# Kernel tuning notes

Measured on AMD Instinct MI355X. Metric: run time of the kernel, lower is better.

## Reference

```python
import jax, jax.numpy as jnp
import numpy as np

NHEAD = 16
EPS_L1 = 1e-12
LN_EPS = 1e-5


def _layernorm(x, g, b):
    mu = jnp.mean(x, axis=-1, keepdims=True)
    var = jnp.mean(jnp.square(x - mu), axis=-1, keepdims=True)
    return (x - mu) / jnp.sqrt(var + LN_EPS) * g + b


def setup_inputs() -> dict:
    key = jax.random.key(0)
    ks = jax.random.split(key, 16)
    S, B, E, P, F = 2048, 2, 1024, 64, 4096
    sc = lambda n: 1.0 / np.sqrt(n)
    return {
        "src": jax.random.normal(ks[0], (S, B, E), jnp.float32),
        "pos_embed": jax.random.normal(ks[1], (B, P, S), jnp.float32),
        "in_proj_w": jax.random.normal(ks[2], (3 * E, E), jnp.float32) * sc(E),
        "in_proj_b": jnp.zeros((3 * E,), jnp.float32),
        "out_w": jax.random.normal(ks[3], (E, E), jnp.float32) * sc(E),
        "out_b": jnp.zeros((E,), jnp.float32),
        "lin1_w": jax.random.normal(ks[4], (F, E), jnp.float32) * sc(E),
        "lin1_b": jnp.zeros((F,), jnp.float32),
        "lin2_w": jax.random.normal(ks[5], (E, F), jnp.float32) * sc(F),
        "lin2_b": jnp.zeros((E,), jnp.float32),
        "ln1_g": jnp.ones((E,), jnp.float32),
        "ln1_b": jnp.zeros((E,), jnp.float32),
        "ln2_g": jnp.ones((E,), jnp.float32),
        "ln2_b": jnp.zeros((E,), jnp.float32),
        "pos_w": jax.random.normal(ks[6], (P, P), jnp.float32) * sc(P),
        "pos_b": jnp.zeros((P,), jnp.float32),
    }


def reference(src, pos_embed, in_proj_w, in_proj_b, out_w, out_b,
              lin1_w, lin1_b, lin2_w, lin2_b,
              ln1_g, ln1_b, ln2_g, ln2_b, pos_w, pos_b):
    S, B, E = src.shape
    H = NHEAD
    Dh = E // H

    # --- custom positional-similarity kernel (cosine_similarity w/ L1 norm) ---
    pe = jnp.einsum('bps,qp->bqs', pos_embed, pos_w) + pos_b[None, :, None]  # learnable pos
    l1 = jnp.maximum(jnp.sum(jnp.abs(pe), axis=1, keepdims=True), EPS_L1)
    pe = pe / l1                                                # [B,P,S]
    pos_sim = jnp.einsum('bps,bpt->bst', pe, pe)                # [B,S,S]

    # --- manual multi-head self-attention ---
    qkv = src @ in_proj_w.T + in_proj_b                          # [S,B,3E]
    q, k, v = jnp.split(qkv, 3, axis=-1)
    q = q * (Dh ** -0.5)
    to_bhsd = lambda t: jnp.transpose(t.reshape(S, B, H, Dh), (1, 2, 0, 3))
    q, k, v = to_bhsd(q), to_bhsd(k), to_bhsd(v)                 # [B,H,S,Dh]
    scores = jnp.einsum('bhsd,bhtd->bhst', q, k) + pos_sim[:, None]
    attn = jax.nn.softmax(scores, axis=-1)                       # [B,H,S,S]
    ctx = jnp.einsum('bhst,bhtd->bhsd', attn, v)                 # [B,H,S,Dh]
    ctx = jnp.transpose(ctx, (2, 0, 1, 3)).reshape(S, B, E)
    attn_out = ctx @ out_w.T + out_b

    # --- residual + norm + FFN (post-norm, relu) ---
    x = _layernorm(src + attn_out, ln1_g, ln1_b)
    ff = jax.nn.relu(x @ lin1_w.T + lin1_b) @ lin2_w.T + lin2_b
    return _layernorm(x + ff, ln2_g, ln2_b)
```

## Files before the change

kernel.cpp:

```cpp
#include <hip/hip_runtime.h>
#include <hip/hip_bf16.h>
#include <math.h>

#define S_LEN 2048
#define BATCH 2
#define EMB   1024
#define NH    16
#define DH    64
#define E3    3072
#define FF    4096
#define PP    64

typedef __bf16 bf16x8 __attribute__((ext_vector_type(8)));
typedef float  floatx4 __attribute__((ext_vector_type(4)));

__device__ __forceinline__ void load_lds16(const void* g, void* l) {
  __builtin_amdgcn_global_load_lds(
      (const __attribute__((address_space(1))) void*)g,
      (__attribute__((address_space(3))) void*)l, 16, 0, 0);
}

__global__ __launch_bounds__(256) void cvt5_kernel(
    const float* __restrict__ in0, __hip_bfloat16* __restrict__ o0,
    const float* __restrict__ in1, __hip_bfloat16* __restrict__ o1,
    const float* __restrict__ in2, __hip_bfloat16* __restrict__ o2,
    const float* __restrict__ in3, __hip_bfloat16* __restrict__ o3,
    const float* __restrict__ in4, __hip_bfloat16* __restrict__ o4)
{
  int bid = blockIdx.x;
  const float* in; __hip_bfloat16* out; int base;
  if      (bid < 2048) { in = in0; out = o0; base = bid; }
  else if (bid < 3584) { in = in1; out = o1; base = bid - 2048; }
  else if (bid < 4096) { in = in2; out = o2; base = bid - 3584; }
  else if (bid < 6144) { in = in3; out = o3; base = bid - 4096; }
  else                 { in = in4; out = o4; base = bid - 6144; }
  int i = (base * 256 + threadIdx.x) * 8;
  float4 a = *(const float4*)&in[i];
  float4 b = *(const float4*)&in[i + 4];
  __hip_bfloat16 t[8];
  t[0] = __float2bfloat16(a.x); t[1] = __float2bfloat16(a.y);
  t[2] = __float2bfloat16(a.z); t[3] = __float2bfloat16(a.w);
  t[4] = __float2bfloat16(b.x); t[5] = __float2bfloat16(b.y);
  t[6] = __float2bfloat16(b.z); t[7] = __float2bfloat16(b.w);
  *(float4*)&out[i] = *(float4*)t;
}

__global__ __launch_bounds__(64) void pe_kernel(
    const float* __restrict__ pos_embed, const float* __restrict__ pos_w,
    const float* __restrict__ pos_b, __hip_bfloat16* __restrict__ peT)
{
  __shared__ float pw[PP * PP];
  int tid = threadIdx.x;
  for (int i = 0; i < PP; ++i) pw[i * PP + tid] = pos_w[i * PP + tid];
  __syncthreads();
  int s = blockIdx.x * 64 + tid;
  int b = blockIdx.y;
  float acc[PP];
#pragma unroll
  for (int q = 0; q < PP; ++q) acc[q] = pos_b[q];
  for (int p = 0; p < PP; ++p) {
    float x = pos_embed[(size_t)(b * PP + p) * S_LEN + s];
#pragma unroll
    for (int q = 0; q < PP; ++q) acc[q] += pw[q * PP + p] * x;
  }
  float l1 = 0.f;
#pragma unroll
  for (int q = 0; q < PP; ++q) l1 += fabsf(acc[q]);
  float inv = 1.f / fmaxf(l1, 1e-12f);
  __hip_bfloat16 tmp[PP];
#pragma unroll
  for (int q = 0; q < PP; ++q) tmp[q] = __float2bfloat16(acc[q] * inv);
  float4* dst = (float4*)&peT[((size_t)b * S_LEN + s) * PP];
#pragma unroll
  for (int i = 0; i < 8; ++i) dst[i] = ((float4*)tmp)[i];
}

template <int WR, int WC>
__global__ __launch_bounds__(256) void gemm_bf16(
    const __hip_bfloat16* __restrict__ A, const __hip_bfloat16* __restrict__ W,
    const float* __restrict__ bias, float* __restrict__ Cf,
    __hip_bfloat16* __restrict__ Cb, int M, int N, int K, int relu, int qkscale,
    long strideA, long strideW, long strideC)
{
  constexpr int BM = 2 * WR * 16;
  constexpr int BN = 2 * WC * 16;
  __shared__ __bf16 As[BM * 64];
  __shared__ __bf16 Bs[BN * 64];
  A += (size_t)blockIdx.z * strideA;
  W += (size_t)blockIdx.z * strideW;
  int tid = threadIdx.x;
  int bm = blockIdx.y * BM;
  int bn = blockIdx.x * BN;
  int wave = tid >> 6, lane = tid & 63;
  int wm = (wave & 1) * (WR * 16), wn = (wave >> 1) * (WC * 16);
  int srow = tid >> 3, scb = tid & 7;
  int gcb = scb ^ (srow & 7);
  const __hip_bfloat16* Ap = A + (size_t)(bm + srow) * K + gcb * 8;
  const __hip_bfloat16* Wp = W + (size_t)(bn + srow) * K + gcb * 8;
  __bf16* AsBase = As + tid * 8;
  __bf16* BsBase = Bs + tid * 8;
  int r15 = lane & 15, quad = lane >> 4;

  floatx4 acc[WR * WC];
#pragma unroll
  for (int i = 0; i < WR * WC; ++i) acc[i] = (floatx4){0.f, 0.f, 0.f, 0.f};

  for (int k0 = 0; k0 < K; k0 += 64) {
    __syncthreads();
#pragma unroll
    for (int io = 0; io < BM / 32; ++io)
      load_lds16(Ap + (size_t)(32 * io) * K + k0, AsBase + io * 2048);
#pragma unroll
    for (int io = 0; io < BN / 32; ++io)
      load_lds16(Wp + (size_t)(32 * io) * K + k0, BsBase + io * 2048);
    __syncthreads();
#pragma unroll
    for (int kc = 0; kc < 2; ++kc) {
      bf16x8 af[WR], bfv[WC];
      int kb = kc * 4 + quad;
#pragma unroll
      for (int i = 0; i < WR; ++i) {
        int rowa = wm + i * 16 + r15;
        af[i] = *(const bf16x8*)&As[rowa * 64 + (kb ^ (rowa & 7)) * 8];
      }
#pragma unroll
      for (int j = 0; j < WC; ++j) {
        int rowb = wn + j * 16 + r15;
        bfv[j] = *(const bf16x8*)&Bs[rowb * 64 + (kb ^ (rowb & 7)) * 8];
      }
#pragma unroll
      for (int i = 0; i < WR; ++i)
#pragma unroll
        for (int j = 0; j < WC; ++j)
          acc[i * WC + j] = __builtin_amdgcn_mfma_f32_16x16x32_bf16(
              af[i], bfv[j], acc[i * WC + j], 0, 0, 0);
    }
  }
  int crow0 = bm + wm + quad * 4;
  int ccol0 = bn + wn + r15;
  float* CfB = Cf ? Cf + (size_t)blockIdx.z * strideC : nullptr;
  __hip_bfloat16* CbB = Cb ? Cb + (size_t)blockIdx.z * strideC : nullptr;
#pragma unroll
  for (int j = 0; j < WC; ++j) {
    int col = ccol0 + j * 16;
    float bv = bias ? bias[col] : 0.f;
    float scale = (qkscale && col < EMB) ? 0.125f : 1.f;
#pragma unroll
    for (int i = 0; i < WR; ++i) {
#pragma unroll
      for (int r = 0; r < 4; ++r) {
        int row = crow0 + i * 16 + r;
        float v = (acc[i * WC + j][r] + bv) * scale;
        if (relu) v = fmaxf(v, 0.f);
        if (CfB) CfB[(size_t)row * N + col] = v;
        if (CbB) CbB[(size_t)row * N + col] = __float2bfloat16(v);
      }
    }
  }
}

__global__ __launch_bounds__(512, 2) void gemm256_bf16(
    const __hip_bfloat16* __restrict__ A, const __hip_bfloat16* __restrict__ W,
    const float* __restrict__ bias, __hip_bfloat16* __restrict__ Cb,
    int M, int N, int K, int relu, int qkscale)
{
  __shared__ __bf16 As[2][16384];
  __shared__ __bf16 Bs[2][16384];
  const int tid = threadIdx.x;
  const int bm = blockIdx.y * 256;
  const int bn = blockIdx.x * 256;
  const int wave = tid >> 6, lane = tid & 63;
  const int wm = (wave >> 2) * 128, wn = (wave & 3) * 64;
  const int r15 = lane & 15, quad = lane >> 4;
  const int srow = tid >> 3, scb = tid & 7;
  const int NT = K >> 6;

  const __hip_bfloat16* Ap = A + (size_t)bm * K;
  const __hip_bfloat16* Wp = W + (size_t)bn * K;

  auto stageA = [&](int buf, int k0, int h) {
#pragma unroll
    for (int io = 0; io < 2; ++io) {
      int row = h * 128 + io * 64 + srow;
      int gcb = scb ^ (row & 7);
      load_lds16(Ap + (size_t)row * K + k0 + gcb * 8,
                 &As[buf][(h * 128 + io * 64) * 64] + tid * 8);
    }
  };
  auto stageB = [&](int buf, int k0, int h) {
#pragma unroll
    for (int io = 0; io < 2; ++io) {
      int row = h * 128 + io * 64 + srow;
      int gcb = scb ^ (row & 7);
      load_lds16(Wp + (size_t)row * K + k0 + gcb * 8,
                 &Bs[buf][(h * 128 + io * 64) * 64] + tid * 8);
    }
  };

  floatx4 acc[8][4];
#pragma unroll
  for (int i = 0; i < 8; ++i)
#pragma unroll
    for (int jn = 0; jn < 4; ++jn) acc[i][jn] = (floatx4){0.f, 0.f, 0.f, 0.f};

  stageA(0, 0, 0); stageA(0, 0, 1);
  stageB(0, 0, 0); stageB(0, 0, 1);
  stageA(1, 64, 0); stageA(1, 64, 1);
  asm volatile("s_waitcnt vmcnt(4)" ::: "memory");
  __builtin_amdgcn_s_barrier();
  __builtin_amdgcn_sched_barrier(0);

#define PHASE_BAR() do { __builtin_amdgcn_sched_barrier(0); \
                         __builtin_amdgcn_s_barrier();      \
                         __builtin_amdgcn_sched_barrier(0); } while (0)

  bf16x8 af[4][2], bfr[4][2];
  for (int j = 0; j < NT; ++j) {
    const int cur = j & 1, nxt = cur ^ 1;
    const int k1 = (j + 1) << 6, k2 = (j + 2) << 6;

#pragma unroll
    for (int i = 0; i < 4; ++i) {
      int row = wm + i * 16 + r15;
#pragma unroll
      for (int kc = 0; kc < 2; ++kc)
        af[i][kc] = *(const bf16x8*)&As[cur][row * 64 + (((kc * 4 + quad) ^ (row & 7)) * 8)];
    }
#pragma unroll
    for (int jn = 0; jn < 2; ++jn) {
      int row = wn + jn * 16 + r15;
#pragma unroll
      for (int kc = 0; kc < 2; ++kc)
        bfr[jn][kc] = *(const bf16x8*)&Bs[cur][row * 64 + (((kc * 4 + quad) ^ (row & 7)) * 8)];
    }
    if (j + 1 < NT) stageB(nxt, k1, 0);
    PHASE_BAR();
    __builtin_amdgcn_s_setprio(1);
#pragma unroll
    for (int i = 0; i < 4; ++i)
#pragma unroll
      for (int jn = 0; jn < 2; ++jn)
#pragma unroll
        for (int kc = 0; kc < 2; ++kc)
          acc[i][jn] = __builtin_amdgcn_mfma_f32_16x16x32_bf16(
              af[i][kc], bfr[jn][kc], acc[i][jn], 0, 0, 0);
    __builtin_amdgcn_s_setprio(0);
    PHASE_BAR();

#pragma unroll
    for (int jn = 2; jn < 4; ++jn) {
      int row = wn + jn * 16 + r15;
#pragma unroll
      for (int kc = 0; kc < 2; ++kc)
        bfr[jn][kc] = *(const bf16x8*)&Bs[cur][row * 64 + (((kc * 4 + quad) ^ (row & 7)) * 8)];
    }
    if (j + 1 < NT) stageB(nxt, k1, 1);
    PHASE_BAR();
    __builtin_amdgcn_s_setprio(1);
#pragma unroll
    for (int i = 0; i < 4; ++i)
#pragma unroll
      for (int jn = 2; jn < 4; ++jn)
#pragma unroll
        for (int kc = 0; kc < 2; ++kc)
          acc[i][jn] = __builtin_amdgcn_mfma_f32_16x16x32_bf16(
              af[i][kc], bfr[jn][kc], acc[i][jn], 0, 0, 0);
    __builtin_amdgcn_s_setprio(0);
    PHASE_BAR();

#pragma unroll
    for (int i = 0; i < 4; ++i) {
      int row = wm + (i + 4) * 16 + r15;
#pragma unroll
      for (int kc = 0; kc < 2; ++kc)
        af[i][kc] = *(const bf16x8*)&As[cur][row * 64 + (((kc * 4 + quad) ^ (row & 7)) * 8)];
    }
    PHASE_BAR();
    __builtin_amdgcn_s_setprio(1);
#pragma unroll
    for (int i = 0; i < 4; ++i)
#pragma unroll
      for (int jn = 2; jn < 4; ++jn)
#pragma unroll
        for (int kc = 0; kc < 2; ++kc)
          acc[i + 4][jn] = __builtin_amdgcn_mfma_f32_16x16x32_bf16(
              af[i][kc], bfr[jn][kc], acc[i + 4][jn], 0, 0, 0);
    __builtin_amdgcn_s_setprio(0);
    PHASE_BAR();

    if (j + 2 < NT) { stageA(cur, k2, 0); stageA(cur, k2, 1); }
    if (j < NT - 2) asm volatile("s_waitcnt vmcnt(4)" ::: "memory");
    else            asm volatile("s_waitcnt vmcnt(0)" ::: "memory");
    PHASE_BAR();
    __builtin_amdgcn_s_setprio(1);
#pragma unroll
    for (int i = 0; i < 4; ++i)
#pragma unroll
      for (int jn = 0; jn < 2; ++jn)
#pragma unroll
        for (int kc = 0; kc < 2; ++kc)
          acc[i + 4][jn] = __builtin_amdgcn_mfma_f32_16x16x32_bf16(
              af[i][kc], bfr[jn][kc], acc[i + 4][jn], 0, 0, 0);
    __builtin_amdgcn_s_setprio(0);
    PHASE_BAR();
  }
#undef PHASE_BAR

  const int crow0 = bm + wm + quad * 4;
  const int ccol0 = bn + wn + r15;
#pragma unroll
  for (int jn = 0; jn < 4; ++jn) {
    int col = ccol0 + jn * 16;
    float bv = bias ? bias[col] : 0.f;
    float scale = (qkscale && col < EMB) ? 0.125f : 1.f;
#pragma unroll
    for (int i = 0; i < 8; ++i) {
#pragma unroll
      for (int r = 0; r < 4; ++r) {
        int row = crow0 + i * 16 + r;
        float v = (acc[i][jn][r] + bv) * scale;
        if (relu) v = fmaxf(v, 0.f);
        Cb[(size_t)row * N + col] = __float2bfloat16(v);
      }
    }
  }
}

__global__ __launch_bounds__(256) void transpose_v(
    const __hip_bfloat16* __restrict__ qkv, __hip_bfloat16* __restrict__ vT)
{
  __shared__ __hip_bfloat16 tile[64][72];
  int c0 = blockIdx.x * 64, t0 = blockIdx.y * 64, b = blockIdx.z;
  int tid = threadIdx.x;
#pragma unroll
  for (int i = 0; i < 2; ++i) {
    int k = tid * 2 + i;
    int row = k >> 3, col = (k & 7) * 8;
    float4 v = *(const float4*)&qkv[((size_t)(t0 + row) * BATCH + b) * E3 + 2 * EMB + c0 + col];
    __hip_bfloat16 tmp[8];
    *(float4*)tmp = v;
#pragma unroll
    for (int j = 0; j < 8; ++j) tile[row][col + j] = tmp[j];
  }
  __syncthreads();
#pragma unroll
  for (int i = 0; i < 2; ++i) {
    int k = tid * 2 + i;
    int crow = k >> 3, tcol = (k & 7) * 8;
    __hip_bfloat16 tmp[8];
#pragma unroll
    for (int j = 0; j < 8; ++j) tmp[j] = tile[tcol + j][crow];
    *(float4*)&vT[((size_t)(b * EMB + c0 + crow)) * S_LEN + t0 + tcol] = *(float4*)tmp;
  }
}

__global__ __launch_bounds__(512, 4) void attn_mfma(
    const __hip_bfloat16* __restrict__ qkv,
    const __hip_bfloat16* __restrict__ vT,
    const __hip_bfloat16* __restrict__ peT,
    __hip_bfloat16* __restrict__ ctx)
{
  __shared__ __bf16 Ks[2][4096];
  __shared__ __bf16 Kp[2][4096];
  __shared__ __bf16 Vs[2][4096];
  __shared__ __bf16 Ps[8192];
  int tid = threadIdx.x;
  int q0 = blockIdx.x * 128, h = blockIdx.y, b = blockIdx.z;
  int w = tid >> 6, lane = tid & 63, quad = lane >> 4, r15 = lane & 15;
  int srow = tid >> 3, scb = tid & 7;
  int x7 = r15 & 7;

  const __hip_bfloat16* kbase = qkv + EMB + (size_t)h * DH;
  const __hip_bfloat16* vbase = vT + ((size_t)b * EMB + h * DH) * S_LEN;
  const __hip_bfloat16* pbase = peT + (size_t)b * S_LEN * PP;

  bf16x8 qa[4];
  {
    int qrow = q0 + w * 16 + r15;
#pragma unroll
    for (int kc = 0; kc < 2; ++kc)
      qa[kc] = *(const bf16x8*)&qkv[
          ((size_t)qrow * BATCH + b) * E3 + h * DH + kc * 32 + quad * 8];
#pragma unroll
    for (int kc = 0; kc < 2; ++kc)
      qa[2 + kc] = *(const bf16x8*)&pbase[
          (size_t)qrow * PP + kc * 32 + quad * 8];
  }

  {
    int row = srow;
    int gcb = scb ^ (row & 7);
    load_lds16(kbase + ((size_t)row * BATCH + b) * E3 + gcb * 8, Ks[0] + tid * 8);
    load_lds16(pbase + (size_t)row * PP + gcb * 8, Kp[0] + tid * 8);
    load_lds16(vbase + (size_t)row * S_LEN + gcb * 8, Vs[0] + tid * 8);
  }
  __syncthreads();

  floatx4 of[4];
#pragma unroll
  for (int j = 0; j < 4; ++j) of[j] = (floatx4){0.f, 0.f, 0.f, 0.f};
  float lp = 0.f;

  __bf16* pw = Ps + w * 1024;

  for (int kt = 0; kt < 32; ++kt) {
    int cur = kt & 1;
    int t0 = kt * 64;
    if (kt < 31) {
      int tn = t0 + 64;
      int nb = cur ^ 1;
      int row = srow;
      int gcb = scb ^ (row & 7);
      load_lds16(kbase + ((size_t)(tn + row) * BATCH + b) * E3 + gcb * 8,
                 Ks[nb] + tid * 8);
      load_lds16(pbase + (size_t)(tn + row) * PP + gcb * 8,
                 Kp[nb] + tid * 8);
      load_lds16(vbase + (size_t)row * S_LEN + tn + gcb * 8,
                 Vs[nb] + tid * 8);
    }

    floatx4 sf[4];
#pragma unroll
    for (int j = 0; j < 4; ++j) sf[j] = (floatx4){0.f, 0.f, 0.f, 0.f};
#pragma unroll
    for (int j = 0; j < 4; ++j) {
      int rowk = j * 16 + r15;
      int rx = rowk & 7;
      bf16x8 kf0 = *(const bf16x8*)&Ks[cur][rowk * 64 + ((quad ^ rx)) * 8];
      bf16x8 kf1 = *(const bf16x8*)&Ks[cur][rowk * 64 + (((4 + quad) ^ rx)) * 8];
      bf16x8 kp0 = *(const bf16x8*)&Kp[cur][rowk * 64 + ((quad ^ rx)) * 8];
      bf16x8 kp1 = *(const bf16x8*)&Kp[cur][rowk * 64 + (((4 + quad) ^ rx)) * 8];
      sf[j] = __builtin_amdgcn_mfma_f32_16x16x32_bf16(kf0, qa[0], sf[j], 0, 0, 0);
      sf[j] = __builtin_amdgcn_mfma_f32_16x16x32_bf16(kf1, qa[1], sf[j], 0, 0, 0);
      sf[j] = __builtin_amdgcn_mfma_f32_16x16x32_bf16(kp0, qa[2], sf[j], 0, 0, 0);
      sf[j] = __builtin_amdgcn_mfma_f32_16x16x32_bf16(kp1, qa[3], sf[j], 0, 0, 0);
    }

#pragma unroll
    for (int j = 0; j < 4; ++j) {
      float e0 = __expf(fminf(sf[j][0], 60.f));
      float e1 = __expf(fminf(sf[j][1], 60.f));
      float e2 = __expf(fminf(sf[j][2], 60.f));
      float e3 = __expf(fminf(sf[j][3], 60.f));
      lp += (e0 + e1) + (e2 + e3);
      __hip_bfloat16 t4[4];
      t4[0] = __float2bfloat16(e0); t4[1] = __float2bfloat16(e1);
      t4[2] = __float2bfloat16(e2); t4[3] = __float2bfloat16(e3);
      int addr = r15 * 64 + (((j * 2 + (quad >> 1)) ^ x7) * 8) + (quad & 1) * 4;
      *(float2*)&pw[addr] = *(float2*)t4;
    }
    __asm__ volatile("s_waitcnt lgkmcnt(0)" ::: "memory");

    bf16x8 pb0 = *(const bf16x8*)&pw[r15 * 64 + ((quad ^ x7) * 8)];
    bf16x8 pb1 = *(const bf16x8*)&pw[r15 * 64 + (((4 + quad) ^ x7) * 8)];
#pragma unroll
    for (int jd = 0; jd < 4; ++jd) {
      int rowd = jd * 16 + r15;
      bf16x8 vb0 = *(const bf16x8*)&Vs[cur][rowd * 64 + (quad ^ (rowd & 7)) * 8];
      bf16x8 vb1 = *(const bf16x8*)&Vs[cur][rowd * 64 + ((4 + quad) ^ (rowd & 7)) * 8];
      of[jd] = __builtin_amdgcn_mfma_f32_16x16x32_bf16(vb0, pb0, of[jd], 0, 0, 0);
      of[jd] = __builtin_amdgcn_mfma_f32_16x16x32_bf16(vb1, pb1, of[jd], 0, 0, 0);
    }
    __syncthreads();
  }

  {
    float l = lp;
    l += __shfl_xor(l, 16, 64);
    l += __shfl_xor(l, 32, 64);
    float inv = 1.f / l;
    size_t rbase = ((size_t)(q0 + w * 16 + r15) * BATCH + b) * EMB + h * DH;
#pragma unroll
    for (int jd = 0; jd < 4; ++jd) {
      __hip_bfloat16 o4[4];
      o4[0] = __float2bfloat16(of[jd][0] * inv);
      o4[1] = __float2bfloat16(of[jd][1] * inv);
      o4[2] = __float2bfloat16(of[jd][2] * inv);
      o4[3] = __float2bfloat16(of[jd][3] * inv);
      *(float2*)&ctx[rbase + jd * 16 + quad * 4] = *(float2*)o4;
    }
  }
}

__global__ __launch_bounds__(256) void ln_kernel(
    const float* __restrict__ x1, const float* __restrict__ x2,
    const float* __restrict__ g, const float* __restrict__ bb,
    float* __restrict__ out, __hip_bfloat16* __restrict__ out_bf)
{
  int row = blockIdx.x;
  int tid = threadIdx.x;
  const float* p1 = x1 + (size_t)row * EMB;
  const float* p2 = x2 + (size_t)row * EMB;
  float4 v1 = *(const float4*)&p1[tid * 4];
  float4 v2 = *(const float4*)&p2[tid * 4];
  float x[4] = {v1.x + v2.x, v1.y + v2.y, v1.z + v2.z, v1.w + v2.w};
  float s = x[0] + x[1] + x[2] + x[3];
  float s2 = x[0] * x[0] + x[1] * x[1] + x[2] * x[2] + x[3] * x[3];
#pragma unroll
  for (int off = 32; off >= 1; off >>= 1) {
    s  += __shfl_xor(s, off, 64);
    s2 += __shfl_xor(s2, off, 64);
  }
  __shared__ float ws1[4], ws2[4];
  int wid = tid >> 6, lane = tid & 63;
  if (lane == 0) { ws1[wid] = s; ws2[wid] = s2; }
  __syncthreads();
  s  = ws1[0] + ws1[1] + ws1[2] + ws1[3];
  s2 = ws2[0] + ws2[1] + ws2[2] + ws2[3];
  float mean = s * (1.f / EMB);
  float var  = s2 * (1.f / EMB) - mean * mean;
  float inv  = rsqrtf(var + 1e-5f);
  float4 gv = *(const float4*)&g[tid * 4];
  float4 bv = *(const float4*)&bb[tid * 4];
  float4 o;
  o.x = (x[0] - mean) * inv * gv.x + bv.x;
  o.y = (x[1] - mean) * inv * gv.y + bv.y;
  o.z = (x[2] - mean) * inv * gv.z + bv.z;
  o.w = (x[3] - mean) * inv * gv.w + bv.w;
  *(float4*)&out[(size_t)row * EMB + tid * 4] = o;
  if (out_bf) {
    __hip_bfloat16 t[4];
    t[0] = __float2bfloat16(o.x); t[1] = __float2bfloat16(o.y);
    t[2] = __float2bfloat16(o.z); t[3] = __float2bfloat16(o.w);
    *(float2*)&out_bf[(size_t)row * EMB + tid * 4] = *(float2*)t;
  }
}

extern "C" void kernel_launch(void* const* d_in, const int* in_sizes, int n_in,
                              void* d_out, int out_size, void* d_ws, size_t ws_size,
                              hipStream_t stream)
{
  const float* src       = (const float*)d_in[0];
  const float* pos_embed = (const float*)d_in[1];
  const float* in_proj_w = (const float*)d_in[2];
  const float* in_proj_b = (const float*)d_in[3];
  const float* out_w     = (const float*)d_in[4];
  const float* out_b     = (const float*)d_in[5];
  const float* lin1_w    = (const float*)d_in[6];
  const float* lin1_b    = (const float*)d_in[7];
  const float* lin2_w    = (const float*)d_in[8];
  const float* lin2_b    = (const float*)d_in[9];
  const float* ln1_g     = (const float*)d_in[10];
  const float* ln1_b     = (const float*)d_in[11];
  const float* ln2_g     = (const float*)d_in[12];
  const float* ln2_b     = (const float*)d_in[13];
  const float* pos_w     = (const float*)d_in[14];
  const float* pos_b     = (const float*)d_in[15];
  float* out = (float*)d_out;
  float* ws  = (float*)d_ws;

  __hip_bfloat16* peT    = (__hip_bfloat16*)ws;
  __hip_bfloat16* qkv_bf = (__hip_bfloat16*)(ws + 8519680);
  __hip_bfloat16* vT_bf  = (__hip_bfloat16*)(ws + 14811136);
  __hip_bfloat16* src_bf = (__hip_bfloat16*)(ws + 16908288);
  __hip_bfloat16* inw_bf  = (__hip_bfloat16*)(ws + 19005440);
  __hip_bfloat16* outw_bf = (__hip_bfloat16*)(ws + 20578304);
  __hip_bfloat16* ctx_bf = (__hip_bfloat16*)(ws + 21102592);
  __hip_bfloat16* l1w_bf = (__hip_bfloat16*)(ws + 23199744);
  __hip_bfloat16* l2w_bf = (__hip_bfloat16*)(ws + 25296896);
  float* proj            = ws + 27394048;
  __hip_bfloat16* x_bf   = (__hip_bfloat16*)ws;
  float* xbuf            = ws + 2097152;
  __hip_bfloat16* h1_bf  = (__hip_bfloat16*)(ws + 6291456);

  const int M = S_LEN * BATCH;

  cvt5_kernel<<<8192, 256, 0, stream>>>(
      src, src_bf, in_proj_w, inw_bf, out_w, outw_bf,
      lin1_w, l1w_bf, lin2_w, l2w_bf);
  pe_kernel<<<dim3(S_LEN / 64, BATCH), 64, 0, stream>>>(pos_embed, pos_w, pos_b, peT);
  gemm256_bf16<<<dim3(E3 / 256, M / 256), 512, 0, stream>>>(
      src_bf, inw_bf, in_proj_b, qkv_bf, M, E3, EMB, 0, 1);
  transpose_v<<<dim3(EMB / 64, S_LEN / 64, BATCH), 256, 0, stream>>>(qkv_bf, vT_bf);
  attn_mfma<<<dim3(S_LEN / 128, NH, BATCH), 512, 0, stream>>>(
      qkv_bf, vT_bf, peT, ctx_bf);
  gemm_bf16<2, 4><<<dim3(EMB / 128, M / 64, 1), 256, 0, stream>>>(
      ctx_bf, outw_bf, out_b, proj, nullptr, M, EMB, EMB, 0, 0, 0, 0, 0);
  ln_kernel<<<dim3(M), 256, 0, stream>>>(src, proj, ln1_g, ln1_b, xbuf, x_bf);
  gemm256_bf16<<<dim3(FF / 256, M / 256), 512, 0, stream>>>(
      x_bf, l1w_bf, lin1_b, h1_bf, M, FF, EMB, 1, 0);
  gemm_bf16<2, 4><<<dim3(EMB / 128, M / 64, 1), 256, 0, stream>>>(
      h1_bf, l2w_bf, lin2_b, proj, nullptr, M, EMB, FF, 0, 0, 0, 0, 0);
  ln_kernel<<<dim3(M), 256, 0, stream>>>(xbuf, proj, ln2_g, ln2_b, out, nullptr);
}
```

Measured before the change: 405.8 us.

## Split-K lin2 GEMM with 3-way LN reduce and exp2-based attention softmax

The FFN second GEMM becomes a 2-way split-K with 128x128 tiles, writing two partial fp32 outputs. A new layernorm kernel sums the residual and both partials, which raises CU occupancy for the K=4096 GEMM at the cost of extra fp32 traffic. The attention softmax now uses exp2 with log2e folded into the Q scale and a pre-scaled positional embedding copy, and the overflow clamp is removed. s_setprio is also added around the MFMA blocks in attention.

```diff
diff --git a/kernel.cpp b/kernel.cpp
--- a/kernel.cpp
+++ b/kernel.cpp
@@ -10,6 +10,8 @@
 #define E3    3072
 #define FF    4096
 #define PP    64
+#define QSCALE 0.18033688f
+#define LOG2E  1.4426950408889634f
 
 typedef __bf16 bf16x8 __attribute__((ext_vector_type(8)));
 typedef float  floatx4 __attribute__((ext_vector_type(4)));
@@ -47,7 +49,8 @@
 
 __global__ __launch_bounds__(64) void pe_kernel(
     const float* __restrict__ pos_embed, const float* __restrict__ pos_w,
-    const float* __restrict__ pos_b, __hip_bfloat16* __restrict__ peT)
+    const float* __restrict__ pos_b, __hip_bfloat16* __restrict__ peT,
+    __hip_bfloat16* __restrict__ peQ)
 {
   __shared__ float pw[PP * PP];
   int tid = threadIdx.x;
@@ -67,12 +70,17 @@
 #pragma unroll
   for (int q = 0; q < PP; ++q) l1 += fabsf(acc[q]);
   float inv = 1.f / fmaxf(l1, 1e-12f);
-  __hip_bfloat16 tmp[PP];
-#pragma unroll
-  for (int q = 0; q < PP; ++q) tmp[q] = __float2bfloat16(acc[q] * inv);
+  __hip_bfloat16 tmp[PP], tmq[PP];
+#pragma unroll
+  for (int q = 0; q < PP; ++q) {
+    float v = acc[q] * inv;
+    tmp[q] = __float2bfloat16(v);
+    tmq[q] = __float2bfloat16(v * LOG2E);
+  }
   float4* dst = (float4*)&peT[((size_t)b * S_LEN + s) * PP];
-#pragma unroll
-  for (int i = 0; i < 8; ++i) dst[i] = ((float4*)tmp)[i];
+  float4* dsq = (float4*)&peQ[((size_t)b * S_LEN + s) * PP];
+#pragma unroll
+  for (int i = 0; i < 8; ++i) { dst[i] = ((float4*)tmp)[i]; dsq[i] = ((float4*)tmq)[i]; }
 }
 
 template <int WR, int WC>
@@ -80,7 +88,7 @@
     const __hip_bfloat16* __restrict__ A, const __hip_bfloat16* __restrict__ W,
     const float* __restrict__ bias, float* __restrict__ Cf,
     __hip_bfloat16* __restrict__ Cb, int M, int N, int K, int relu, int qkscale,
-    long strideA, long strideW, long strideC)
+    int ldA, int ldW, long strideA, long strideW, long strideC)
 {
   constexpr int BM = 2 * WR * 16;
   constexpr int BN = 2 * WC * 16;
@@ -95,8 +103,8 @@
   int wm = (wave & 1) * (WR * 16), wn = (wave >> 1) * (WC * 16);
   int srow = tid >> 3, scb = tid & 7;
   int gcb = scb ^ (srow & 7);
-  const __hip_bfloat16* Ap = A + (size_t)(bm + srow) * K + gcb * 8;
-  const __hip_bfloat16* Wp = W + (size_t)(bn + srow) * K + gcb * 8;
+  const __hip_bfloat16* Ap = A + (size_t)(bm + srow) * ldA + gcb * 8;
+  const __hip_bfloat16* Wp = W + (size_t)(bn + srow) * ldW + gcb * 8;
   __bf16* AsBase = As + tid * 8;
   __bf16* BsBase = Bs + tid * 8;
   int r15 = lane & 15, quad = lane >> 4;
@@ -109,10 +117,10 @@
     __syncthreads();
 #pragma unroll
     for (int io = 0; io < BM / 32; ++io)
-      load_lds16(Ap + (size_t)(32 * io) * K + k0, AsBase + io * 2048);
+      load_lds16(Ap + (size_t)(32 * io) * ldA + k0, AsBase + io * 2048);
 #pragma unroll
     for (int io = 0; io < BN / 32; ++io)
-      load_lds16(Wp + (size_t)(32 * io) * K + k0, BsBase + io * 2048);
+      load_lds16(Wp + (size_t)(32 * io) * ldW + k0, BsBase + io * 2048);
     __syncthreads();
 #pragma unroll
     for (int kc = 0; kc < 2; ++kc) {
@@ -138,13 +146,13 @@
   }
   int crow0 = bm + wm + quad * 4;
   int ccol0 = bn + wn + r15;
-  float* CfB = Cf ? Cf + (size_t)blockIdx.z * strideC : nullptr;
-  __hip_bfloat16* CbB = Cb ? Cb + (size_t)blockIdx.z * strideC : nullptr;
+  float* CfB = Cf ? Cf + (long)blockIdx.z * strideC : nullptr;
+  __hip_bfloat16* CbB = Cb;
 #pragma unroll
   for (int j = 0; j < WC; ++j) {
     int col = ccol0 + j * 16;
-    float bv = bias ? bias[col] : 0.f;
-    float scale = (qkscale && col < EMB) ? 0.125f : 1.f;
+    float bv = (bias && blockIdx.z == 0) ? bias[col] : 0.f;
+    float scale = (qkscale && col < EMB) ? QSCALE : 1.f;
 #pragma unroll
     for (int i = 0; i < WR; ++i) {
 #pragma unroll
@@ -312,7 +320,7 @@
   for (int jn = 0; jn < 4; ++jn) {
     int col = ccol0 + jn * 16;
     float bv = bias ? bias[col] : 0.f;
-    float scale = (qkscale && col < EMB) ? 0.125f : 1.f;
+    float scale = (qkscale && col < EMB) ? QSCALE : 1.f;
 #pragma unroll
     for (int i = 0; i < 8; ++i) {
 #pragma unroll
@@ -358,6 +366,7 @@
     const __hip_bfloat16* __restrict__ qkv,
     const __hip_bfloat16* __restrict__ vT,
     const __hip_bfloat16* __restrict__ peT,
+    const __hip_bfloat16* __restrict__ peQ,
     __hip_bfloat16* __restrict__ ctx)
 {
   __shared__ __bf16 Ks[2][4096];
@@ -372,7 +381,8 @@
 
   const __hip_bfloat16* kbase = qkv + EMB + (size_t)h * DH;
   const __hip_bfloat16* vbase = vT + ((size_t)b * EMB + h * DH) * S_LEN;
-  const __hip_bfloat16* pbase = peT + (size_t)b * S_LEN * PP;
+  const __hip_bfloat16* pkbase = peT + (size_t)b * S_LEN * PP;
+  const __hip_bfloat16* pqbase = peQ + (size_t)b * S_LEN * PP;
 
   bf16x8 qa[4];
   {
@@ -383,7 +393,7 @@
           ((size_t)qrow * BATCH + b) * E3 + h * DH + kc * 32 + quad * 8];
 #pragma unroll
     for (int kc = 0; kc < 2; ++kc)
-      qa[2 + kc] = *(const bf16x8*)&pbase[
+      qa[2 + kc] = *(const bf16x8*)&pqbase[
           (size_t)qrow * PP + kc * 32 + quad * 8];
   }
 
@@ -391,7 +401,7 @@
     int row = srow;
     int gcb = scb ^ (row & 7);
     load_lds16(kbase + ((size_t)row * BATCH + b) * E3 + gcb * 8, Ks[0] + tid * 8);
-    load_lds16(pbase + (size_t)row * PP + gcb * 8, Kp[0] + tid * 8);
+    load_lds16(pkbase + (size_t)row * PP + gcb * 8, Kp[0] + tid * 8);
     load_lds16(vbase + (size_t)row * S_LEN + gcb * 8, Vs[0] + tid * 8);
   }
   __syncthreads();
@@ -413,7 +423,7 @@
       int gcb = scb ^ (row & 7);
       load_lds16(kbase + ((size_t)(tn + row) * BATCH + b) * E3 + gcb * 8,
                  Ks[nb] + tid * 8);
-      load_lds16(pbase + (size_t)(tn + row) * PP + gcb * 8,
+      load_lds16(pkbase + (size_t)(tn + row) * PP + gcb * 8,
                  Kp[nb] + tid * 8);
       load_lds16(vbase + (size_t)row * S_LEN + tn + gcb * 8,
                  Vs[nb] + tid * 8);
@@ -422,6 +432,7 @@
     floatx4 sf[4];
 #pragma unroll
     for (int j = 0; j < 4; ++j) sf[j] = (floatx4){0.f, 0.f, 0.f, 0.f};
+    __builtin_amdgcn_s_setprio(1);
 #pragma unroll
     for (int j = 0; j < 4; ++j) {
       int rowk = j * 16 + r15;
@@ -435,13 +446,14 @@
       sf[j] = __builtin_amdgcn_mfma_f32_16x16x32_bf16(kp0, qa[2], sf[j], 0, 0, 0);
       sf[j] = __builtin_amdgcn_mfma_f32_16x16x32_bf16(kp1, qa[3], sf[j], 0, 0, 0);
     }
+    __builtin_amdgcn_s_setprio(0);
 
 #pragma unroll
     for (int j = 0; j < 4; ++j) {
-      float e0 = __expf(fminf(sf[j][0], 60.f));
-      float e1 = __expf(fminf(sf[j][1], 60.f));
-      float e2 = __expf(fminf(sf[j][2], 60.f));
-      float e3 = __expf(fminf(sf[j][3], 60.f));
+      float e0 = exp2f(sf[j][0]);
+      float e1 = exp2f(sf[j][1]);
+      float e2 = exp2f(sf[j][2]);
+      float e3 = exp2f(sf[j][3]);
       lp += (e0 + e1) + (e2 + e3);
       __hip_bfloat16 t4[4];
       t4[0] = __float2bfloat16(e0); t4[1] = __float2bfloat16(e1);
@@ -453,6 +465,7 @@
 
     bf16x8 pb0 = *(const bf16x8*)&pw[r15 * 64 + ((quad ^ x7) * 8)];
     bf16x8 pb1 = *(const bf16x8*)&pw[r15 * 64 + (((4 + quad) ^ x7) * 8)];
+    __builtin_amdgcn_s_setprio(1);
 #pragma unroll
     for (int jd = 0; jd < 4; ++jd) {
       int rowd = jd * 16 + r15;
@@ -461,6 +474,7 @@
       of[jd] = __builtin_amdgcn_mfma_f32_16x16x32_bf16(vb0, pb0, of[jd], 0, 0, 0);
       of[jd] = __builtin_amdgcn_mfma_f32_16x16x32_bf16(vb1, pb1, of[jd], 0, 0, 0);
     }
+    __builtin_amdgcn_s_setprio(0);
     __syncthreads();
   }
 
@@ -526,6 +540,48 @@
   }
 }
 
+__global__ __launch_bounds__(256) void ln3_kernel(
+    const float* __restrict__ x1, const float* __restrict__ x2,
+    const float* __restrict__ x3,
+    const float* __restrict__ g, const float* __restrict__ bb,
+    float* __restrict__ out)
+{
+  int row = blockIdx.x;
+  int tid = threadIdx.x;
+  const float* p1 = x1 + (size_t)row * EMB;
+  const float* p2 = x2 + (size_t)row * EMB;
+  const float* p3 = x3 + (size_t)row * EMB;
+  float4 v1 = *(const float4*)&p1[tid * 4];
+  float4 v2 = *(const float4*)&p2[tid * 4];
+  float4 v3 = *(const float4*)&p3[tid * 4];
+  float x[4] = {v1.x + v2.x + v3.x, v1.y + v2.y + v3.y,
+                v1.z + v2.z + v3.z, v1.w + v2.w + v3.w};
+  float s = x[0] + x[1] + x[2] + x[3];
+  float s2 = x[0] * x[0] + x[1] * x[1] + x[2] * x[2] + x[3] * x[3];
+#pragma unroll
+  for (int off = 32; off >= 1; off >>= 1) {
+    s  += __shfl_xor(s, off, 64);
+    s2 += __shfl_xor(s2, off, 64);
+  }
+  __shared__ float ws1[4], ws2[4];
+  int wid = tid >> 6, lane = tid & 63;
+  if (lane == 0) { ws1[wid] = s; ws2[wid] = s2; }
+  __syncthreads();
+  s  = ws1[0] + ws1[1] + ws1[2] + ws1[3];
+  s2 = ws2[0] + ws2[1] + ws2[2] + ws2[3];
+  float mean = s * (1.f / EMB);
+  float var  = s2 * (1.f / EMB) - mean * mean;
+  float inv  = rsqrtf(var + 1e-5f);
+  float4 gv = *(const float4*)&g[tid * 4];
+  float4 bv = *(const float4*)&bb[tid * 4];
+  float4 o;
+  o.x = (x[0] - mean) * inv * gv.x + bv.x;
+  o.y = (x[1] - mean) * inv * gv.y + bv.y;
+  o.z = (x[2] - mean) * inv * gv.z + bv.z;
+  o.w = (x[3] - mean) * inv * gv.w + bv.w;
+  *(float4*)&out[(size_t)row * EMB + tid * 4] = o;
+}
+
 extern "C" void kernel_launch(void* const* d_in, const int* in_sizes, int n_in,
                               void* d_out, int out_size, void* d_ws, size_t ws_size,
                               hipStream_t stream)
@@ -550,6 +606,7 @@
   float* ws  = (float*)d_ws;
 
   __hip_bfloat16* peT    = (__hip_bfloat16*)ws;
+  __hip_bfloat16* peQ    = (__hip_bfloat16*)(ws + 131072);
   __hip_bfloat16* qkv_bf = (__hip_bfloat16*)(ws + 8519680);
   __hip_bfloat16* vT_bf  = (__hip_bfloat16*)(ws + 14811136);
   __hip_bfloat16* src_bf = (__hip_bfloat16*)(ws + 16908288);
@@ -562,24 +619,26 @@
   __hip_bfloat16* x_bf   = (__hip_bfloat16*)ws;
   float* xbuf            = ws + 2097152;
   __hip_bfloat16* h1_bf  = (__hip_bfloat16*)(ws + 6291456);
+  float* proj2           = ws + 14811136;
 
   const int M = S_LEN * BATCH;
 
   cvt5_kernel<<<8192, 256, 0, stream>>>(
       src, src_bf, in_proj_w, inw_bf, out_w, outw_bf,
       lin1_w, l1w_bf, lin2_w, l2w_bf);
-  pe_kernel<<<dim3(S_LEN / 64, BATCH), 64, 0, stream>>>(pos_embed, pos_w, pos_b, peT);
+  pe_kernel<<<dim3(S_LEN / 64, BATCH), 64, 0, stream>>>(pos_embed, pos_w, pos_b, peT, peQ);
   gemm256_bf16<<<dim3(E3 / 256, M / 256), 512, 0, stream>>>(
       src_bf, inw_bf, in_proj_b, qkv_bf, M, E3, EMB, 0, 1);
   transpose_v<<<dim3(EMB / 64, S_LEN / 64, BATCH), 256, 0, stream>>>(qkv_bf, vT_bf);
   attn_mfma<<<dim3(S_LEN / 128, NH, BATCH), 512, 0, stream>>>(
-      qkv_bf, vT_bf, peT, ctx_bf);
+      qkv_bf, vT_bf, peT, peQ, ctx_bf);
   gemm_bf16<2, 4><<<dim3(EMB / 128, M / 64, 1), 256, 0, stream>>>(
-      ctx_bf, outw_bf, out_b, proj, nullptr, M, EMB, EMB, 0, 0, 0, 0, 0);
+      ctx_bf, outw_bf, out_b, proj, nullptr, M, EMB, EMB, 0, 0, EMB, EMB, 0, 0, 0);
   ln_kernel<<<dim3(M), 256, 0, stream>>>(src, proj, ln1_g, ln1_b, xbuf, x_bf);
   gemm256_bf16<<<dim3(FF / 256, M / 256), 512, 0, stream>>>(
       x_bf, l1w_bf, lin1_b, h1_bf, M, FF, EMB, 1, 0);
-  gemm_bf16<2, 4><<<dim3(EMB / 128, M / 64, 1), 256, 0, stream>>>(
-      h1_bf, l2w_bf, lin2_b, proj, nullptr, M, EMB, FF, 0, 0, 0, 0, 0);
-  ln_kernel<<<dim3(M), 256, 0, stream>>>(xbuf, proj, ln2_g, ln2_b, out, nullptr);
-}
+  gemm_bf16<4, 4><<<dim3(EMB / 128, M / 128, 2), 256, 0, stream>>>(
+      h1_bf, l2w_bf, lin2_b, proj, nullptr, M, EMB, FF / 2, 0, 0,
+      FF, FF, FF / 2, FF / 2, (long)(proj2 - proj));
+  ln3_kernel<<<dim3(M), 256, 0, stream>>>(xbuf, proj, proj2, ln2_g, ln2_b, out);
+}
```

Result: no change. 411.0 us (+1.3%).
